# Performance work log

Measured on AMD Instinct MI355X. Metric: run time of the kernel, lower is better.

The kernel has to match this reference:

```python
import jax, jax.numpy as jnp
import numpy as np
import math

B, S, D = 2, 2048, 2048
HQ, HKV = 16, 4            # query heads, kv heads
HD = D // HQ               # head dim = 128
REPS = HQ // HKV           # queries per kv head = 4
KVD = HKV * HD             # 512


def setup_inputs() -> dict:
    key = jax.random.key(0)
    ks = jax.random.split(key, 7)
    s = 0.02
    return {
        "hidden_states": jax.random.normal(ks[0], (B, S, D), dtype=jnp.float32),
        "Wq": jax.random.normal(ks[1], (D, D), dtype=jnp.float32) * s,
        "bq": jnp.zeros((D,), dtype=jnp.float32),
        "Wk": jax.random.normal(ks[2], (D, KVD), dtype=jnp.float32) * s,
        "bk": jnp.zeros((KVD,), dtype=jnp.float32),
        "Wv": jax.random.normal(ks[3], (D, KVD), dtype=jnp.float32) * s,
        "bv": jnp.zeros((KVD,), dtype=jnp.float32),
    }


def reference(hidden_states, Wq, bq, Wk, bk, Wv, bv):
    b, s, d = hidden_states.shape
    # Projections
    q = hidden_states @ Wq + bq                      # [B,S,D]
    k = hidden_states @ Wk + bk                      # [B,S,KVD]
    v = hidden_states @ Wv + bv                      # [B,S,KVD]
    # Split heads. torch repeat_kv_heads uses .repeat (tile), so expanded
    # head h maps to kv head (h mod HKV). Reshape q heads as (REPS, HKV)
    # so axis g indexes the kv head, matching that tiling exactly.
    q = q.reshape(b, s, HQ, HD).transpose(0, 2, 1, 3)          # [B,HQ,S,hd]
    q = q.reshape(b, REPS, HKV, s, HD)                          # [B,R,G,S,hd]
    k = k.reshape(b, s, HKV, HD).transpose(0, 2, 1, 3)          # [B,G,S,hd]
    v = v.reshape(b, s, HKV, HD).transpose(0, 2, 1, 3)          # [B,G,S,hd]
    scale = 1.0 / math.sqrt(HD)
    scores = jnp.einsum('brgsd,bgtd->brgst', q, k) * scale      # [B,R,G,S,S]
    probs = jax.nn.softmax(scores, axis=-1)
    ctx = jnp.einsum('brgst,bgtd->brgsd', probs, v)             # [B,R,G,S,hd]
    ctx = ctx.reshape(b, HQ, s, HD).transpose(0, 2, 1, 3)       # [B,S,HQ,hd]
    return ctx.reshape(b, s, HQ * HD)                            # [B,S,D]
```

## Files before the change

### kernel.cpp

```cpp
#include <hip/hip_runtime.h>
#include <hip/hip_bf16.h>

#define QSCALE   0.08838834764831845f
#define QKSCALE  0.1275174468755322f

typedef __attribute__((ext_vector_type(8))) short bh8;
typedef __attribute__((ext_vector_type(4))) float fx4;
typedef __attribute__((ext_vector_type(4))) short sh4;

typedef const __attribute__((address_space(1))) unsigned GAu;
typedef __attribute__((address_space(3))) unsigned LAu;

__device__ __forceinline__ short f2bf(float f) {
    unsigned u = __float_as_uint(f);
    unsigned r = u + 0x7fffu + ((u >> 16) & 1u);
    return (short)(r >> 16);
}

__device__ __forceinline__ unsigned pk_bf16(float x, float y) {
    union { __hip_bfloat162 h; unsigned u; } cv;
    cv.h = __float22bfloat162_rn(float2{x, y});
    return cv.u;
}

__global__ __launch_bounds__(256) void cvt_x(const float* __restrict__ x,
                                             short* __restrict__ o) {
    int i = blockIdx.x * 256 + threadIdx.x;
    float4 v = ((const float4*)x)[i];
    sh4 s;
    s.x = f2bf(v.x); s.y = f2bf(v.y); s.z = f2bf(v.z); s.w = f2bf(v.w);
    ((sh4*)o)[i] = s;
}

__global__ __launch_bounds__(256) void transpose_w(const float* __restrict__ w,
                                                   short* __restrict__ wt,
                                                   int K, int N) {
    __shared__ float tile[32][33];
    int nb = blockIdx.x, kb = blockIdx.y;
    int tx = threadIdx.x & 31, ty = threadIdx.x >> 5;
#pragma unroll
    for (int j = 0; j < 4; ++j) {
        int k = kb * 32 + ty + j * 8;
        tile[ty + j * 8][tx] = w[(size_t)k * N + nb * 32 + tx];
    }
    __syncthreads();
#pragma unroll
    for (int j = 0; j < 4; ++j) {
        int n = nb * 32 + ty + j * 8;
        wt[(size_t)n * K + kb * 32 + tx] = f2bf(tile[tx][ty + j * 8]);
    }
}

__global__ __launch_bounds__(256) void proj_gemm(
    const short* __restrict__ X,
    const short* __restrict__ WqT,
    const short* __restrict__ WkT,
    const short* __restrict__ WvT,
    const float* __restrict__ bq, const float* __restrict__ bk,
    const float* __restrict__ bv,
    short* __restrict__ Qb, short* __restrict__ Kpk, short* __restrict__ Vpk) {
    __shared__ short As0[128 * 32];
    __shared__ short As1[128 * 32];
    __shared__ short Bs0[128 * 32];
    __shared__ short Bs1[128 * 32];

    const int tid = threadIdx.x;
    const int bm = blockIdx.x;
    const int ntg = blockIdx.y;

    const short* Wm; const float* bias; int col0, kind;
    if (ntg < 16)      { Wm = WqT; bias = bq; col0 = ntg * 128;        kind = 0; }
    else if (ntg < 20) { Wm = WkT; bias = bk; col0 = (ntg - 16) * 128; kind = 1; }
    else               { Wm = WvT; bias = bv; col0 = (ntg - 20) * 128; kind = 2; }

    const int w = tid >> 6, lane = tid & 63, quad = lane >> 4, l16 = lane & 15;

    fx4 acc[2][8];
#pragma unroll
    for (int i = 0; i < 2; ++i)
#pragma unroll
        for (int j = 0; j < 8; ++j) acc[i][j] = fx4{0.f, 0.f, 0.f, 0.f};

    const int srow = w * 16 + (lane >> 2);
    const int scol = (((lane & 3) ^ ((lane >> 2) & 3)) * 8);
    const short* Ag = X + (size_t)(bm * 128 + srow) * 2048 + scol;
    const short* Bg = Wm + (size_t)(col0 + srow) * 2048 + scol;
    const int stoff = w * 512;

    const int fchunk = (quad ^ (l16 & 3)) * 8;
    const int aoff0 = (w * 32 + l16) * 32 + fchunk;
    const int aoff1 = aoff0 + 512;
    const int boff  = l16 * 32 + fchunk;

    const short* pA00 = As0 + aoff0;  const short* pA01 = As0 + aoff1;
    const short* pA10 = As1 + aoff0;  const short* pA11 = As1 + aoff1;
    const short* pB0  = Bs0 + boff;   const short* pB1  = Bs1 + boff;

#define PG_STAGE(AsD, BsD, ktile)                                               \
    do {                                                                        \
        const int k0_ = (ktile) * 32;                                           \
        _Pragma("unroll")                                                       \
        for (int j = 0; j < 2; ++j) {                                           \
            __builtin_amdgcn_global_load_lds(                                   \
                (GAu*)(Ag + (size_t)(j * 64) * 2048 + k0_),                     \
                (LAu*)(AsD + stoff + j * 2048), 16, 0, 0);                      \
            __builtin_amdgcn_global_load_lds(                                   \
                (GAu*)(Bg + (size_t)(j * 64) * 2048 + k0_),                     \
                (LAu*)(BsD + stoff + j * 2048), 16, 0, 0);                      \
        }                                                                       \
    } while (0)

#define PG_COMPUTE(pA0_, pA1_, pB_)                                             \
    do {                                                                        \
        bh8 af0 = *(const bh8*)(pA0_);                                          \
        bh8 af1 = *(const bh8*)(pA1_);                                          \
        _Pragma("unroll")                                                       \
        for (int nt = 0; nt < 8; ++nt) {                                        \
            bh8 bf = *(const bh8*)((pB_) + nt * 512);                           \
            acc[0][nt] = __builtin_amdgcn_mfma_f32_16x16x32_bf16(af0, bf, acc[0][nt], 0, 0, 0); \
            acc[1][nt] = __builtin_amdgcn_mfma_f32_16x16x32_bf16(af1, bf, acc[1][nt], 0, 0, 0); \
        }                                                                       \
    } while (0)

    PG_STAGE(As0, Bs0, 0);
    __syncthreads();

    for (int kt = 0; kt < 64; kt += 2) {
        PG_STAGE(As1, Bs1, kt + 1);
        PG_COMPUTE(pA00, pA01, pB0);
        __syncthreads();

        if (kt < 62) PG_STAGE(As0, Bs0, kt + 2);
        PG_COMPUTE(pA10, pA11, pB1);
        __syncthreads();
    }
#undef PG_STAGE
#undef PG_COMPUTE

#pragma unroll
    for (int mt = 0; mt < 2; ++mt) {
        int srow2 = bm * 128 + w * 32 + mt * 16 + quad * 4;
#pragma unroll
        for (int nt = 0; nt < 8; ++nt) {
            int c = col0 + nt * 16 + l16;
            float bval = bias[c];
#pragma unroll
            for (int r = 0; r < 4; ++r) {
                int sg = srow2 + r;
                int b = sg >> 11, s = sg & 2047;
                float v = acc[mt][nt][r] + bval;
                int hd = c & 127;
                if (kind == 0) {
                    v *= QKSCALE;
                    int h = c >> 7;
                    Qb[(((size_t)(b * 16 + h) * 2048 + s) << 7) + hd] = f2bf(v);
                } else if (kind == 1) {
                    int g = c >> 7;
                    int ktt = s >> 6, tl = s & 63;
                    int fnt = tl >> 4, fl16 = tl & 15;
                    int ks = hd >> 5, qd = (hd >> 3) & 3, j = hd & 7;
                    size_t frag = (((size_t)(b * 4 + g) * 32 + ktt) * 16 + fnt * 4 + ks);
                    Kpk[frag * 512 + (qd * 16 + fl16) * 8 + j] = f2bf(v);
                } else {
                    int g = c >> 7;
                    int ktt = s >> 6, tl = s & 63;
                    int ts = tl >> 5, qd = (tl >> 3) & 3, j = tl & 7;
                    int fnt = hd >> 4, fl16 = hd & 15;
                    size_t frag = (((size_t)(b * 4 + g) * 32 + ktt) * 16 + fnt * 2 + ts);
                    Vpk[frag * 512 + (qd * 16 + fl16) * 8 + j] = f2bf(v);
                }
            }
        }
    }
}

__global__ __launch_bounds__(256, 4) void attn(
    const short* __restrict__ Qb,
    const short* __restrict__ Kpk,
    const short* __restrict__ Vpk,
    float* __restrict__ out) {
    __shared__ short Ks0[8 * 512];
    __shared__ short Ks1[8 * 512];
    __shared__ short Vs0[8 * 512];
    __shared__ short Vs1[8 * 512];
    __shared__ __align__(16) unsigned Ps[4][16][20];

    const int bid = blockIdx.x;
    const int gb = bid & 7;
    const int rep = (bid >> 3) & 3;
    const int qt = bid >> 5;
    const int b = gb >> 2, g = gb & 3;
    const int h = rep * 4 + g;
    const int tid = threadIdx.x, w = tid >> 6, lane = tid & 63;
    const int quad = lane >> 4, l16 = lane & 15;

    bh8 qf[4];
    {
        int s = qt * 64 + w * 16 + l16;
        const short* qp = Qb + (((size_t)(b * 16 + h) * 2048 + s) << 7);
#pragma unroll
        for (int ks = 0; ks < 4; ++ks)
            qf[ks] = *(const bh8*)(qp + ks * 32 + quad * 8);
    }

    const short* kbase = Kpk + ((size_t)gb * 32) * 8192;
    const short* vbase = Vpk + ((size_t)gb * 32) * 8192;

    const short* pK0 = Ks0 + lane * 8;
    const short* pK1 = Ks1 + lane * 8;
    const short* pV0 = Vs0 + lane * 8;
    const short* pV1 = Vs1 + lane * 8;

    fx4 ctx[8];
#pragma unroll
    for (int j = 0; j < 8; ++j) ctx[j] = fx4{0.f, 0.f, 0.f, 0.f};
    float l_part[4] = {0.f, 0.f, 0.f, 0.f};

#define AT_STAGE(KsD, VsD, kn)                                                  \
    do {                                                                        \
        const short* kp_ = kbase + (size_t)(kn) * 4096;                         \
        const short* vp_ = vbase + (size_t)((kn) >> 1) * 8192 + ((kn) & 1) * 512;\
        _Pragma("unroll")                                                       \
        for (int i = 0; i < 2; ++i) {                                           \
            int f = w * 2 + i;                                                  \
            __builtin_amdgcn_global_load_lds((GAu*)(kp_ + f * 512 + lane * 8),  \
                                             (LAu*)(KsD + f * 512), 16, 0, 0);  \
            __builtin_amdgcn_global_load_lds((GAu*)(vp_ + (size_t)f * 1024 + lane * 8),\
                                             (LAu*)(VsD + f * 512), 16, 0, 0);  \
        }                                                                       \
    } while (0)

#define AT_COMPUTE(pKC, pVC)                                                    \
    do {                                                                        \
        fx4 sc0 = fx4{0.f, 0.f, 0.f, 0.f};                                      \
        fx4 sc1 = fx4{0.f, 0.f, 0.f, 0.f};                                      \
        _Pragma("unroll")                                                       \
        for (int ks = 0; ks < 4; ++ks) {                                        \
            bh8 kf = *(const bh8*)((pKC) + ks * 512);                           \
            sc0 = __builtin_amdgcn_mfma_f32_16x16x32_bf16(qf[ks], kf, sc0, 0, 0, 0); \
        }                                                                       \
        _Pragma("unroll")                                                       \
        for (int ks = 0; ks < 4; ++ks) {                                        \
            bh8 kf = *(const bh8*)((pKC) + (4 + ks) * 512);                     \
            sc1 = __builtin_amdgcn_mfma_f32_16x16x32_bf16(qf[ks], kf, sc1, 0, 0, 0); \
        }                                                                       \
        _Pragma("unroll")                                                       \
        for (int r = 0; r < 4; ++r) {                                           \
            float p0 = __builtin_amdgcn_exp2f(sc0[r]);                          \
            float p1 = __builtin_amdgcn_exp2f(sc1[r]);                          \
            l_part[r] += p0 + p1;                                               \
            Ps[w][quad * 4 + r][l16] = pk_bf16(p0, p1);                         \
        }                                                                       \
        bh8 pa;                                                                 \
        {                                                                       \
            const unsigned* prow = &Ps[w][l16][(quad & 1) * 8];                 \
            uint4 lo = *(const uint4*)(prow);                                   \
            uint4 hi = *(const uint4*)(prow + 4);                               \
            unsigned dw[8] = {lo.x, lo.y, lo.z, lo.w, hi.x, hi.y, hi.z, hi.w};  \
            unsigned sel = (quad & 2) ? 0x07060302u : 0x05040100u;              \
            unsigned a[4];                                                      \
            _Pragma("unroll")                                                   \
            for (int j = 0; j < 4; ++j)                                         \
                a[j] = __builtin_amdgcn_perm(dw[2 * j + 1], dw[2 * j], sel);    \
            pa = *(const bh8*)a;                                                \
        }                                                                       \
        _Pragma("unroll")                                                       \
        for (int nt = 0; nt < 8; ++nt) {                                        \
            bh8 vf = *(const bh8*)((pVC) + nt * 512);                           \
            ctx[nt] = __builtin_amdgcn_mfma_f32_16x16x32_bf16(pa, vf, ctx[nt], 0, 0, 0); \
        }                                                                       \
    } while (0)

    AT_STAGE(Ks0, Vs0, 0);
    __syncthreads();

    for (int kt = 0; kt < 64; kt += 2) {
        AT_STAGE(Ks1, Vs1, kt + 1);
        AT_COMPUTE(pK0, pV0);
        __syncthreads();

        if (kt < 62) AT_STAGE(Ks0, Vs0, kt + 2);
        AT_COMPUTE(pK1, pV1);
        __syncthreads();
    }
#undef AT_STAGE
#undef AT_COMPUTE

    {
        int srow = qt * 64 + w * 16 + quad * 4;
#pragma unroll
        for (int r = 0; r < 4; ++r) {
            float lsum = l_part[r];
            lsum += __shfl_xor(lsum, 1);
            lsum += __shfl_xor(lsum, 2);
            lsum += __shfl_xor(lsum, 4);
            lsum += __shfl_xor(lsum, 8);
            float inv = 1.f / lsum;
            size_t rowoff = ((size_t)b * 2048 + (srow + r)) * 2048 + h * 128;
#pragma unroll
            for (int nt = 0; nt < 8; ++nt)
                out[rowoff + nt * 16 + l16] = ctx[nt][r] * inv;
        }
    }
}

extern "C" void kernel_launch(void* const* d_in, const int* in_sizes, int n_in,
                              void* d_out, int out_size, void* d_ws, size_t ws_size,
                              hipStream_t stream) {
    const float* hs = (const float*)d_in[0];
    const float* Wq = (const float*)d_in[1];
    const float* bq = (const float*)d_in[2];
    const float* Wk = (const float*)d_in[3];
    const float* bk = (const float*)d_in[4];
    const float* Wv = (const float*)d_in[5];
    const float* bv = (const float*)d_in[6];
    float* out = (float*)d_out;

    char* ws = (char*)d_ws;
    short* Xbf = (short*)(ws);
    short* WqT = (short*)(ws + 16777216);
    short* WkT = (short*)(ws + 25165824);
    short* WvT = (short*)(ws + 27262976);
    short* Qb  = (short*)(ws + 29360128);
    short* Kpk = (short*)(ws + 46137344);
    short* Vpk = (short*)(ws + 50331648);

    cvt_x<<<8192, 256, 0, stream>>>(hs, Xbf);
    transpose_w<<<dim3(64, 64), 256, 0, stream>>>(Wq, WqT, 2048, 2048);
    transpose_w<<<dim3(16, 64), 256, 0, stream>>>(Wk, WkT, 2048, 512);
    transpose_w<<<dim3(16, 64), 256, 0, stream>>>(Wv, WvT, 2048, 512);
    proj_gemm<<<dim3(32, 24), 256, 0, stream>>>(Xbf, WqT, WkT, WvT, bq, bk, bv,
                                                Qb, Kpk, Vpk);
    attn<<<1024, 256, 0, stream>>>(Qb, Kpk, Vpk, out);
}
```

Baseline: 277.2 us.

## Process two 16-row query groups per wave in attention, halving waves per block

The attention block now runs 2 waves of 128 threads instead of 4, and each wave handles 32 query rows as two 16-row groups. Each K and V fragment read from LDS then feeds two MFMAs, halving LDS traffic per unit of compute. Each wave also issues twice as many global-to-LDS loads per stage. The cost is roughly double the accumulator and Q registers per wave and fewer waves per block to hide latency, with launch bounds relaxed to allow the extra registers.

```diff
diff --git a/kernel.cpp b/kernel.cpp
--- a/kernel.cpp
+++ b/kernel.cpp
@@ -174,7 +174,7 @@
     }
 }
 
-__global__ __launch_bounds__(256, 4) void attn(
+__global__ __launch_bounds__(128, 2) void attn(
     const short* __restrict__ Qb,
     const short* __restrict__ Kpk,
     const short* __restrict__ Vpk,
@@ -183,7 +183,7 @@
     __shared__ short Ks1[8 * 512];
     __shared__ short Vs0[8 * 512];
     __shared__ short Vs1[8 * 512];
-    __shared__ __align__(16) unsigned Ps[4][16][20];
+    __shared__ __align__(16) unsigned Ps[2][32][20];
 
     const int bid = blockIdx.x;
     const int gb = bid & 7;
@@ -194,13 +194,14 @@
     const int tid = threadIdx.x, w = tid >> 6, lane = tid & 63;
     const int quad = lane >> 4, l16 = lane & 15;
 
-    bh8 qf[4];
-    {
-        int s = qt * 64 + w * 16 + l16;
+    bh8 qf[2][4];
+#pragma unroll
+    for (int rg = 0; rg < 2; ++rg) {
+        int s = qt * 64 + w * 32 + rg * 16 + l16;
         const short* qp = Qb + (((size_t)(b * 16 + h) * 2048 + s) << 7);
 #pragma unroll
         for (int ks = 0; ks < 4; ++ks)
-            qf[ks] = *(const bh8*)(qp + ks * 32 + quad * 8);
+            qf[rg][ks] = *(const bh8*)(qp + ks * 32 + quad * 8);
     }
 
     const short* kbase = Kpk + ((size_t)gb * 32) * 8192;
@@ -211,18 +212,20 @@
     const short* pV0 = Vs0 + lane * 8;
     const short* pV1 = Vs1 + lane * 8;
 
-    fx4 ctx[8];
-#pragma unroll
-    for (int j = 0; j < 8; ++j) ctx[j] = fx4{0.f, 0.f, 0.f, 0.f};
-    float l_part[4] = {0.f, 0.f, 0.f, 0.f};
+    fx4 ctx[2][8];
+#pragma unroll
+    for (int rg = 0; rg < 2; ++rg)
+#pragma unroll
+        for (int j = 0; j < 8; ++j) ctx[rg][j] = fx4{0.f, 0.f, 0.f, 0.f};
+    float l_part[2][4] = {{0.f, 0.f, 0.f, 0.f}, {0.f, 0.f, 0.f, 0.f}};
 
 #define AT_STAGE(KsD, VsD, kn)                                                  \
     do {                                                                        \
         const short* kp_ = kbase + (size_t)(kn) * 4096;                         \
         const short* vp_ = vbase + (size_t)((kn) >> 1) * 8192 + ((kn) & 1) * 512;\
         _Pragma("unroll")                                                       \
-        for (int i = 0; i < 2; ++i) {                                           \
-            int f = w * 2 + i;                                                  \
+        for (int i = 0; i < 4; ++i) {                                           \
+            int f = w * 4 + i;                                                  \
             __builtin_amdgcn_global_load_lds((GAu*)(kp_ + f * 512 + lane * 8),  \
                                              (LAu*)(KsD + f * 512), 16, 0, 0);  \
             __builtin_amdgcn_global_load_lds((GAu*)(vp_ + (size_t)f * 1024 + lane * 8),\
@@ -232,28 +235,32 @@
 
 #define AT_COMPUTE(pKC, pVC)                                                    \
     do {                                                                        \
-        fx4 sc0 = fx4{0.f, 0.f, 0.f, 0.f};                                      \
-        fx4 sc1 = fx4{0.f, 0.f, 0.f, 0.f};                                      \
-        _Pragma("unroll")                                                       \
-        for (int ks = 0; ks < 4; ++ks) {                                        \
-            bh8 kf = *(const bh8*)((pKC) + ks * 512);                           \
-            sc0 = __builtin_amdgcn_mfma_f32_16x16x32_bf16(qf[ks], kf, sc0, 0, 0, 0); \
-        }                                                                       \
-        _Pragma("unroll")                                                       \
-        for (int ks = 0; ks < 4; ++ks) {                                        \
-            bh8 kf = *(const bh8*)((pKC) + (4 + ks) * 512);                     \
-            sc1 = __builtin_amdgcn_mfma_f32_16x16x32_bf16(qf[ks], kf, sc1, 0, 0, 0); \
-        }                                                                       \
-        _Pragma("unroll")                                                       \
-        for (int r = 0; r < 4; ++r) {                                           \
-            float p0 = __builtin_amdgcn_exp2f(sc0[r]);                          \
-            float p1 = __builtin_amdgcn_exp2f(sc1[r]);                          \
-            l_part[r] += p0 + p1;                                               \
-            Ps[w][quad * 4 + r][l16] = pk_bf16(p0, p1);                         \
-        }                                                                       \
-        bh8 pa;                                                                 \
-        {                                                                       \
-            const unsigned* prow = &Ps[w][l16][(quad & 1) * 8];                 \
+        fx4 sc[2][2];                                                           \
+        sc[0][0] = fx4{0.f, 0.f, 0.f, 0.f}; sc[0][1] = fx4{0.f, 0.f, 0.f, 0.f}; \
+        sc[1][0] = fx4{0.f, 0.f, 0.f, 0.f}; sc[1][1] = fx4{0.f, 0.f, 0.f, 0.f}; \
+        _Pragma("unroll")                                                       \
+        for (int nti = 0; nti < 2; ++nti) {                                     \
+            _Pragma("unroll")                                                   \
+            for (int ks = 0; ks < 4; ++ks) {                                    \
+                bh8 kf = *(const bh8*)((pKC) + (nti * 4 + ks) * 512);           \
+                sc[0][nti] = __builtin_amdgcn_mfma_f32_16x16x32_bf16(qf[0][ks], kf, sc[0][nti], 0, 0, 0); \
+                sc[1][nti] = __builtin_amdgcn_mfma_f32_16x16x32_bf16(qf[1][ks], kf, sc[1][nti], 0, 0, 0); \
+            }                                                                   \
+        }                                                                       \
+        _Pragma("unroll")                                                       \
+        for (int rg = 0; rg < 2; ++rg) {                                        \
+            _Pragma("unroll")                                                   \
+            for (int r = 0; r < 4; ++r) {                                       \
+                float p0 = __builtin_amdgcn_exp2f(sc[rg][0][r]);                \
+                float p1 = __builtin_amdgcn_exp2f(sc[rg][1][r]);                \
+                l_part[rg][r] += p0 + p1;                                       \
+                Ps[w][rg * 16 + quad * 4 + r][l16] = pk_bf16(p0, p1);           \
+            }                                                                   \
+        }                                                                       \
+        bh8 pa[2];                                                              \
+        _Pragma("unroll")                                                       \
+        for (int rg = 0; rg < 2; ++rg) {                                        \
+            const unsigned* prow = &Ps[w][rg * 16 + l16][(quad & 1) * 8];       \
             uint4 lo = *(const uint4*)(prow);                                   \
             uint4 hi = *(const uint4*)(prow + 4);                               \
             unsigned dw[8] = {lo.x, lo.y, lo.z, lo.w, hi.x, hi.y, hi.z, hi.w};  \
@@ -262,12 +269,13 @@
             _Pragma("unroll")                                                   \
             for (int j = 0; j < 4; ++j)                                         \
                 a[j] = __builtin_amdgcn_perm(dw[2 * j + 1], dw[2 * j], sel);    \
-            pa = *(const bh8*)a;                                                \
+            pa[rg] = *(const bh8*)a;                                            \
         }                                                                       \
         _Pragma("unroll")                                                       \
         for (int nt = 0; nt < 8; ++nt) {                                        \
             bh8 vf = *(const bh8*)((pVC) + nt * 512);                           \
-            ctx[nt] = __builtin_amdgcn_mfma_f32_16x16x32_bf16(pa, vf, ctx[nt], 0, 0, 0); \
+            ctx[0][nt] = __builtin_amdgcn_mfma_f32_16x16x32_bf16(pa[0], vf, ctx[0][nt], 0, 0, 0); \
+            ctx[1][nt] = __builtin_amdgcn_mfma_f32_16x16x32_bf16(pa[1], vf, ctx[1][nt], 0, 0, 0); \
         }                                                                       \
     } while (0)
 
@@ -286,11 +294,12 @@
 #undef AT_STAGE
 #undef AT_COMPUTE
 
-    {
-        int srow = qt * 64 + w * 16 + quad * 4;
+#pragma unroll
+    for (int rg = 0; rg < 2; ++rg) {
+        int srow = qt * 64 + w * 32 + rg * 16 + quad * 4;
 #pragma unroll
         for (int r = 0; r < 4; ++r) {
-            float lsum = l_part[r];
+            float lsum = l_part[rg][r];
             lsum += __shfl_xor(lsum, 1);
             lsum += __shfl_xor(lsum, 2);
             lsum += __shfl_xor(lsum, 4);
@@ -299,7 +308,7 @@
             size_t rowoff = ((size_t)b * 2048 + (srow + r)) * 2048 + h * 128;
 #pragma unroll
             for (int nt = 0; nt < 8; ++nt)
-                out[rowoff + nt * 16 + l16] = ctx[nt][r] * inv;
+                out[rowoff + nt * 16 + l16] = ctx[rg][nt][r] * inv;
         }
     }
 }
@@ -331,5 +340,5 @@
     transpose_w<<<dim3(16, 64), 256, 0, stream>>>(Wv, WvT, 2048, 512);
     proj_gemm<<<dim3(32, 24), 256, 0, stream>>>(Xbf, WqT, WkT, WvT, bq, bk, bv,
                                                 Qb, Kpk, Vpk);
-    attn<<<1024, 256, 0, stream>>>(Qb, Kpk, Vpk, out);
-}
+    attn<<<1024, 128, 0, stream>>>(Qb, Kpk, Vpk, out);
+}
```

After: 267.1 us. -3.6%, faster.
